# Kernel tuning notes

Measured on AMD Instinct MI355X. Metric: run time of the kernel, lower is better.

The kernel has to match this reference:

```python
import jax, jax.numpy as jnp
import numpy as np

IN_F, OUT_F, RANK = 4096, 4096, 4
ALPHA = 16
SCALING = ALPHA / RANK  # 4.0
B, L = 2, 4096


def setup_inputs() -> dict:
    key = jax.random.key(0)
    k_x, k_w, k_a, k_b = jax.random.split(key, 4)
    x = jax.random.normal(k_x, (B, L, IN_F), dtype=jnp.float32)
    W = jax.random.normal(k_w, (OUT_F, IN_F), dtype=jnp.float32) * 0.02
    # module inits lora_A ~ N(0, 1/rank), lora_B = zeros; we use small random B
    # so the low-rank branch is numerically active for kernel testing.
    lora_A = jax.random.normal(k_a, (RANK, IN_F), dtype=jnp.float32) * (1.0 / RANK)
    lora_B = jax.random.normal(k_b, (OUT_F, RANK), dtype=jnp.float32) * 0.02
    return {"x": x, "W": W, "lora_A": lora_A, "lora_B": lora_B}


def reference(x, W, lora_A, lora_B):
    # out = x @ W.T + ((x @ A.T) @ B.T) * scaling
    original = jnp.einsum('bli,oi->blo', x, W)
    lora_a = jnp.einsum('bli,ri->blr', x, lora_A)      # [B,L,rank]
    lora = jnp.einsum('blr,or->blo', lora_a, lora_B)   # [B,L,out]
    return original + lora * SCALING
```

## Files before the change

### kernel.cpp

```cpp
#include <hip/hip_runtime.h>
#include <stdint.h>

typedef signed char i8;
typedef unsigned char u8;
typedef __attribute__((ext_vector_type(4))) int i32x4;
typedef __attribute__((ext_vector_type(4))) float f32x4;

__device__ __forceinline__ void gload_lds16(const void* g, void* l) {
  __builtin_amdgcn_global_load_lds(
      (__attribute__((address_space(1))) void*)const_cast<void*>(g),
      (__attribute__((address_space(3))) void*)l, 16, 0, 0);
}

__global__ __launch_bounds__(256) void k_quant_x(const float* __restrict__ in,
                                                 i8* __restrict__ out,
                                                 float* __restrict__ scale) {
  const int row = blockIdx.x, t = threadIdx.x;
  const float* src = in + (size_t)row * 4096;
  float4 v[4];
  float m = 0.f;
#pragma unroll
  for (int j = 0; j < 4; ++j) {
    v[j] = *(const float4*)(src + j * 1024 + t * 4);
    m = fmaxf(m, fmaxf(fmaxf(fabsf(v[j].x), fabsf(v[j].y)),
                       fmaxf(fabsf(v[j].z), fabsf(v[j].w))));
  }
#pragma unroll
  for (int off = 32; off; off >>= 1) m = fmaxf(m, __shfl_xor(m, off));
  __shared__ float wmax[4];
  if ((t & 63) == 0) wmax[t >> 6] = m;
  __syncthreads();
  m = fmaxf(fmaxf(wmax[0], wmax[1]), fmaxf(wmax[2], wmax[3]));
  const float inv = m > 0.f ? 127.f / m : 0.f;
  if (t == 0) scale[row] = m / 127.f;
#pragma unroll
  for (int j = 0; j < 4; ++j) {
    int q0 = (int)rintf(fmaxf(fminf(v[j].x * inv, 127.f), -127.f));
    int q1 = (int)rintf(fmaxf(fminf(v[j].y * inv, 127.f), -127.f));
    int q2 = (int)rintf(fmaxf(fminf(v[j].z * inv, 127.f), -127.f));
    int q3 = (int)rintf(fmaxf(fminf(v[j].w * inv, 127.f), -127.f));
    uint32_t p = (q0 & 255) | ((q1 & 255) << 8) | ((q2 & 255) << 16) | ((q3 & 255) << 24);
    *(uint32_t*)(out + (size_t)row * 4096 + j * 1024 + t * 4) = p;
  }
}

__global__ __launch_bounds__(256) void k_quant_w(const float* __restrict__ W,
                                                 const float* __restrict__ Am,
                                                 const float* __restrict__ Bm,
                                                 i8* __restrict__ out,
                                                 float* __restrict__ scale) {
  const int o = blockIdx.x, t = threadIdx.x;
  const float4 b4 = *(const float4*)(Bm + (o << 2));
  float4 v[4];
  float m = 0.f;
#pragma unroll
  for (int j = 0; j < 4; ++j) {
    const int i = j * 1024 + t * 4;
    float4 w  = *(const float4*)(W + ((size_t)o << 12) + i);
    float4 a0 = *(const float4*)(Am + i);
    float4 a1 = *(const float4*)(Am + 4096 + i);
    float4 a2 = *(const float4*)(Am + 8192 + i);
    float4 a3 = *(const float4*)(Am + 12288 + i);
    w.x += 4.f * (b4.x * a0.x + b4.y * a1.x + b4.z * a2.x + b4.w * a3.x);
    w.y += 4.f * (b4.x * a0.y + b4.y * a1.y + b4.z * a2.y + b4.w * a3.y);
    w.z += 4.f * (b4.x * a0.z + b4.y * a1.z + b4.z * a2.z + b4.w * a3.z);
    w.w += 4.f * (b4.x * a0.w + b4.y * a1.w + b4.z * a2.w + b4.w * a3.w);
    v[j] = w;
    m = fmaxf(m, fmaxf(fmaxf(fabsf(w.x), fabsf(w.y)), fmaxf(fabsf(w.z), fabsf(w.w))));
  }
#pragma unroll
  for (int off = 32; off; off >>= 1) m = fmaxf(m, __shfl_xor(m, off));
  __shared__ float wmax[4];
  if ((t & 63) == 0) wmax[t >> 6] = m;
  __syncthreads();
  m = fmaxf(fmaxf(wmax[0], wmax[1]), fmaxf(wmax[2], wmax[3]));
  const float inv = m > 0.f ? 127.f / m : 0.f;
  if (t == 0) scale[o] = m / 127.f;
#pragma unroll
  for (int j = 0; j < 4; ++j) {
    int q0 = (int)rintf(fmaxf(fminf(v[j].x * inv, 127.f), -127.f));
    int q1 = (int)rintf(fmaxf(fminf(v[j].y * inv, 127.f), -127.f));
    int q2 = (int)rintf(fmaxf(fminf(v[j].z * inv, 127.f), -127.f));
    int q3 = (int)rintf(fmaxf(fminf(v[j].w * inv, 127.f), -127.f));
    uint32_t p = (q0 & 255) | ((q1 & 255) << 8) | ((q2 & 255) << 16) | ((q3 & 255) << 24);
    *(uint32_t*)(out + (size_t)o * 4096 + j * 1024 + t * 4) = p;
  }
}

__global__ __launch_bounds__(512, 2) void k_gq8(const u8* __restrict__ Ag,
                                                const u8* __restrict__ Bg,
                                                const float* __restrict__ sx,
                                                const float* __restrict__ sw,
                                                float* __restrict__ C,
                                                int M, int N, int K) {
  __shared__ __attribute__((aligned(16))) u8 As[2 * 32768];
  __shared__ __attribute__((aligned(16))) u8 Bs[2 * 32768];
  const int tid  = threadIdx.x;
  const int wave = tid >> 6, lane = tid & 63;
  const int wr = wave >> 2, wc = wave & 3;
  const int m0 = blockIdx.y * 256, n0 = blockIdx.x * 256;
  const int NT = K >> 7;

  const int srow = tid >> 3;
  const int csrc = (tid & 7) ^ (srow & 7);
  const u8* pA = Ag + (size_t)(m0 + srow) * K + csrc * 16;
  const u8* pB = Bg + (size_t)(n0 + srow) * K + csrc * 16;
  const size_t KH = (size_t)128 * K;
  const size_t KU = (size_t)64 * K;
  const int wb = wave << 10;

#define SA(nb, h, kt)                                                          \
  do {                                                                         \
    gload_lds16(pA + (h) * KH + (kt),      As + (nb) * 32768 + (h) * 16384 + wb);       \
    gload_lds16(pA + (h) * KH + KU + (kt), As + (nb) * 32768 + (h) * 16384 + 8192 + wb);\
  } while (0)
#define SB(nb, h, kt)                                                          \
  do {                                                                         \
    gload_lds16(pB + (h) * KH + (kt),      Bs + (nb) * 32768 + (h) * 16384 + wb);       \
    gload_lds16(pB + (h) * KH + KU + (kt), Bs + (nb) * 32768 + (h) * 16384 + 8192 + wb);\
  } while (0)

  const int l4 = lane & 15, q = lane >> 4, l7 = lane & 7;
  const int ke0 = (q ^ l7) << 4;
  const int aoff = ((wr << 6) + l4) << 7;
  const int boff = ((wc << 5) + l4) << 7;

  i32x4 acc[8][4] = {};
  i32x4 ar[4][2];
  i32x4 bq[2][2][2];

#define LDA(buf, mh)                                                           \
  do {                                                                         \
    const u8* b_ = As + (buf) * 32768 + (mh) * 16384 + aoff;                   \
    _Pragma("unroll") for (int f = 0; f < 4; ++f) {                            \
      ar[f][0] = *(const i32x4*)(b_ + f * 2048 + ke0);                         \
      ar[f][1] = *(const i32x4*)(b_ + f * 2048 + (ke0 ^ 64));                  \
    }                                                                          \
  } while (0)
#define LDB(buf, nh)                                                           \
  do {                                                                         \
    const u8* b_ = Bs + (buf) * 32768 + (nh) * 16384 + boff;                   \
    _Pragma("unroll") for (int g = 0; g < 2; ++g) {                            \
      bq[nh][g][0] = *(const i32x4*)(b_ + g * 2048 + ke0);                     \
      bq[nh][g][1] = *(const i32x4*)(b_ + g * 2048 + (ke0 ^ 64));              \
    }                                                                          \
  } while (0)
#define MFMA16(mh, nh)                                                         \
  do {                                                                         \
    __builtin_amdgcn_s_setprio(1);                                             \
    _Pragma("unroll") for (int f = 0; f < 4; ++f)                              \
      _Pragma("unroll") for (int g = 0; g < 2; ++g)                            \
        _Pragma("unroll") for (int ks = 0; ks < 2; ++ks)                       \
          acc[(mh) * 4 + f][(nh) * 2 + g] =                                    \
              __builtin_amdgcn_mfma_i32_16x16x64_i8(                           \
                  ar[f][ks], bq[nh][g][ks], acc[(mh) * 4 + f][(nh) * 2 + g],   \
                  0, 0, 0);                                                    \
    __builtin_amdgcn_s_setprio(0);                                             \
  } while (0)

  SA(0, 0, 0);
  SB(0, 0, 0);
  SB(0, 1, 0);
  SA(0, 1, 0);
  asm volatile("s_waitcnt vmcnt(4)" ::: "memory");
  __builtin_amdgcn_s_barrier();

  for (int t = 0; t < NT; ++t) {
    const int buf = t & 1, nb = buf ^ 1;
    const int kt1 = (t + 1) << 7;
    const bool st = (t + 1) < NT;

    LDA(buf, 0);
    LDB(buf, 0);
    if (st) SA(nb, 0, kt1);
    asm volatile("s_waitcnt lgkmcnt(8)" ::: "memory");
    __builtin_amdgcn_s_barrier();
    asm volatile("s_waitcnt lgkmcnt(0)" ::: "memory");
    MFMA16(0, 0);
    if (st) { asm volatile("s_waitcnt vmcnt(4)" ::: "memory"); }
    else    { asm volatile("s_waitcnt vmcnt(2)" ::: "memory"); }
    __builtin_amdgcn_s_barrier();

    LDB(buf, 1);
    if (st) SB(nb, 0, kt1);
    __builtin_amdgcn_s_barrier();
    asm volatile("s_waitcnt lgkmcnt(0)" ::: "memory");
    MFMA16(0, 1);
    if (st) { asm volatile("s_waitcnt vmcnt(4)" ::: "memory"); }
    else    { asm volatile("s_waitcnt vmcnt(0)" ::: "memory"); }
    __builtin_amdgcn_s_barrier();

    LDA(buf, 1);
    if (st) SB(nb, 1, kt1);
    __builtin_amdgcn_s_barrier();
    asm volatile("s_waitcnt lgkmcnt(0)" ::: "memory");
    MFMA16(1, 1);
    __builtin_amdgcn_s_barrier();

    if (st) SA(nb, 1, kt1);
    __builtin_amdgcn_s_barrier();
    MFMA16(1, 0);
    if (st) { asm volatile("s_waitcnt vmcnt(4)" ::: "memory"); }
    __builtin_amdgcn_s_barrier();
  }

  float swv[4];
#pragma unroll
  for (int j = 0; j < 4; ++j)
    swv[j] = sw[n0 + (j >> 1) * 128 + wc * 32 + (j & 1) * 16 + l4];
#pragma unroll
  for (int i = 0; i < 8; ++i) {
    const int mh = i >> 2, f = i & 3;
    const int row = m0 + mh * 128 + wr * 64 + f * 16 + q * 4;
#pragma unroll
    for (int j = 0; j < 4; ++j) {
      const int nh = j >> 1, g = j & 1;
      const int col = n0 + nh * 128 + wc * 32 + g * 16 + l4;
#pragma unroll
      for (int v = 0; v < 4; ++v)
        C[(size_t)(row + v) * N + col] = (float)acc[i][j][v] * sx[row + v] * swv[j];
    }
  }
#undef SA
#undef SB
#undef LDA
#undef LDB
#undef MFMA16
}

__global__ __launch_bounds__(256) void k_fallback(const float* __restrict__ X,
                                                  const float* __restrict__ W,
                                                  const float* __restrict__ Am,
                                                  const float* __restrict__ Bm,
                                                  float* __restrict__ C,
                                                  int M, int N, int K) {
  __shared__ float Xs[64][16];
  __shared__ float Ws[64][17];
  const int tid = threadIdx.x;
  const int tn = tid & 15, tm = tid >> 4;
  const int m0 = blockIdx.y * 64, n0 = blockIdx.x * 64;
  float acc[4][4] = {};
  for (int kt = 0; kt < K; kt += 16) {
    __syncthreads();
#pragma unroll
    for (int qq = 0; qq < 4; ++qq) {
      int idx = qq * 256 + tid;
      int r = idx >> 4, c = idx & 15;
      Xs[r][c] = X[(size_t)(m0 + r) * K + kt + c];
      float w = W[(size_t)(n0 + r) * K + kt + c];
      float4 b = *(const float4*)(Bm + ((n0 + r) << 2));
      w += 4.f * (b.x * Am[kt + c] + b.y * Am[4096 + kt + c] +
                  b.z * Am[8192 + kt + c] + b.w * Am[12288 + kt + c]);
      Ws[r][c] = w;
    }
    __syncthreads();
#pragma unroll
    for (int k = 0; k < 16; ++k) {
      float xv[4], wv[4];
#pragma unroll
      for (int i = 0; i < 4; ++i) xv[i] = Xs[tm * 4 + i][k];
#pragma unroll
      for (int j = 0; j < 4; ++j) wv[j] = Ws[tn * 4 + j][k];
#pragma unroll
      for (int i = 0; i < 4; ++i)
#pragma unroll
        for (int j = 0; j < 4; ++j) acc[i][j] += xv[i] * wv[j];
    }
  }
#pragma unroll
  for (int i = 0; i < 4; ++i)
#pragma unroll
    for (int j = 0; j < 4; ++j)
      C[(size_t)(m0 + tm * 4 + i) * N + n0 + tn * 4 + j] = acc[i][j];
}

extern "C" void kernel_launch(void* const* d_in, const int* in_sizes, int n_in,
                              void* d_out, int out_size, void* d_ws, size_t ws_size,
                              hipStream_t stream) {
  const float* x  = (const float*)d_in[0];
  const float* W  = (const float*)d_in[1];
  const float* lA = (const float*)d_in[2];
  const float* lB = (const float*)d_in[3];
  float* out = (float*)d_out;
  const int K = 4096, N = 4096;
  const int M = in_sizes[0] / K;
  const size_t need = (size_t)(M + N) * K + (size_t)(M + N) * sizeof(float);

  if (ws_size >= need && (M % 256) == 0) {
    i8* xb = (i8*)d_ws;
    i8* wb = xb + (size_t)M * K;
    float* sx = (float*)(wb + (size_t)N * K);
    float* sw = sx + M;
    k_quant_x<<<dim3(M), dim3(256), 0, stream>>>(x, xb, sx);
    k_quant_w<<<dim3(N), dim3(256), 0, stream>>>(W, lA, lB, wb, sw);
    k_gq8<<<dim3(N / 256, M / 256), dim3(512), 0, stream>>>(
        (const u8*)xb, (const u8*)wb, sx, sw, out, M, N, K);
  } else {
    k_fallback<<<dim3(N / 64, M / 64), dim3(256), 0, stream>>>(x, W, lA, lB, out, M, N, K);
  }
}
```

Measured before the change: 194.4 us.

## Merge x and W quantization kernels and swizzle GEMM workgroups across XCDs

Combines the separate activation and weight quantization kernels into one launch whose blocks branch on block index, removing one kernel launch and the tail gap between the two. The int8 GEMM now remaps its linear workgroup id so consecutive ids are spread in chunks of eight, aiming to place neighbouring tiles on the same XCD for better L2 reuse of shared A/B rows. A divisibility-by-eight guard is added to the fast path. The branchy fused quant kernel adds some divergence per block but no per-thread divergence.

```diff
diff --git a/kernel.cpp b/kernel.cpp
--- a/kernel.cpp
+++ b/kernel.cpp
@@ -4,7 +4,6 @@
 typedef signed char i8;
 typedef unsigned char u8;
 typedef __attribute__((ext_vector_type(4))) int i32x4;
-typedef __attribute__((ext_vector_type(4))) float f32x4;
 
 __device__ __forceinline__ void gload_lds16(const void* g, void* l) {
   __builtin_amdgcn_global_load_lds(
@@ -12,18 +11,44 @@
       (__attribute__((address_space(3))) void*)l, 16, 0, 0);
 }
 
-__global__ __launch_bounds__(256) void k_quant_x(const float* __restrict__ in,
-                                                 i8* __restrict__ out,
-                                                 float* __restrict__ scale) {
-  const int row = blockIdx.x, t = threadIdx.x;
-  const float* src = in + (size_t)row * 4096;
+__global__ __launch_bounds__(256) void k_quant(const float* __restrict__ x,
+                                               const float* __restrict__ W,
+                                               const float* __restrict__ Am,
+                                               const float* __restrict__ Bm,
+                                               i8* __restrict__ xq,
+                                               i8* __restrict__ wq,
+                                               float* __restrict__ sx,
+                                               float* __restrict__ sw, int M) {
+  const int bid = blockIdx.x, t = threadIdx.x;
+  const bool isx = bid < M;
+  const int row = isx ? bid : bid - M;
   float4 v[4];
   float m = 0.f;
-#pragma unroll
-  for (int j = 0; j < 4; ++j) {
-    v[j] = *(const float4*)(src + j * 1024 + t * 4);
-    m = fmaxf(m, fmaxf(fmaxf(fabsf(v[j].x), fabsf(v[j].y)),
-                       fmaxf(fabsf(v[j].z), fabsf(v[j].w))));
+  if (isx) {
+    const float4* src = (const float4*)(x + (size_t)row * 4096);
+#pragma unroll
+    for (int j = 0; j < 4; ++j) {
+      v[j] = src[j * 256 + t];
+      m = fmaxf(m, fmaxf(fmaxf(fabsf(v[j].x), fabsf(v[j].y)),
+                         fmaxf(fabsf(v[j].z), fabsf(v[j].w))));
+    }
+  } else {
+    const float4 b4 = *(const float4*)(Bm + (row << 2));
+#pragma unroll
+    for (int j = 0; j < 4; ++j) {
+      const int i = (j * 256 + t) * 4;
+      float4 w  = *(const float4*)(W + ((size_t)row << 12) + i);
+      float4 a0 = *(const float4*)(Am + i);
+      float4 a1 = *(const float4*)(Am + 4096 + i);
+      float4 a2 = *(const float4*)(Am + 8192 + i);
+      float4 a3 = *(const float4*)(Am + 12288 + i);
+      w.x += 4.f * (b4.x * a0.x + b4.y * a1.x + b4.z * a2.x + b4.w * a3.x);
+      w.y += 4.f * (b4.x * a0.y + b4.y * a1.y + b4.z * a2.y + b4.w * a3.y);
+      w.z += 4.f * (b4.x * a0.z + b4.y * a1.z + b4.z * a2.z + b4.w * a3.z);
+      w.w += 4.f * (b4.x * a0.w + b4.y * a1.w + b4.z * a2.w + b4.w * a3.w);
+      v[j] = w;
+      m = fmaxf(m, fmaxf(fmaxf(fabsf(w.x), fabsf(w.y)), fmaxf(fabsf(w.z), fabsf(w.w))));
+    }
   }
 #pragma unroll
   for (int off = 32; off; off >>= 1) m = fmaxf(m, __shfl_xor(m, off));
@@ -32,7 +57,8 @@
   __syncthreads();
   m = fmaxf(fmaxf(wmax[0], wmax[1]), fmaxf(wmax[2], wmax[3]));
   const float inv = m > 0.f ? 127.f / m : 0.f;
-  if (t == 0) scale[row] = m / 127.f;
+  if (t == 0) { if (isx) sx[row] = m / 127.f; else sw[row] = m / 127.f; }
+  i8* out = isx ? xq : wq;
 #pragma unroll
   for (int j = 0; j < 4; ++j) {
     int q0 = (int)rintf(fmaxf(fminf(v[j].x * inv, 127.f), -127.f));
@@ -40,50 +66,7 @@
     int q2 = (int)rintf(fmaxf(fminf(v[j].z * inv, 127.f), -127.f));
     int q3 = (int)rintf(fmaxf(fminf(v[j].w * inv, 127.f), -127.f));
     uint32_t p = (q0 & 255) | ((q1 & 255) << 8) | ((q2 & 255) << 16) | ((q3 & 255) << 24);
-    *(uint32_t*)(out + (size_t)row * 4096 + j * 1024 + t * 4) = p;
-  }
-}
-
-__global__ __launch_bounds__(256) void k_quant_w(const float* __restrict__ W,
-                                                 const float* __restrict__ Am,
-                                                 const float* __restrict__ Bm,
-                                                 i8* __restrict__ out,
-                                                 float* __restrict__ scale) {
-  const int o = blockIdx.x, t = threadIdx.x;
-  const float4 b4 = *(const float4*)(Bm + (o << 2));
-  float4 v[4];
-  float m = 0.f;
-#pragma unroll
-  for (int j = 0; j < 4; ++j) {
-    const int i = j * 1024 + t * 4;
-    float4 w  = *(const float4*)(W + ((size_t)o << 12) + i);
-    float4 a0 = *(const float4*)(Am + i);
-    float4 a1 = *(const float4*)(Am + 4096 + i);
-    float4 a2 = *(const float4*)(Am + 8192 + i);
-    float4 a3 = *(const float4*)(Am + 12288 + i);
-    w.x += 4.f * (b4.x * a0.x + b4.y * a1.x + b4.z * a2.x + b4.w * a3.x);
-    w.y += 4.f * (b4.x * a0.y + b4.y * a1.y + b4.z * a2.y + b4.w * a3.y);
-    w.z += 4.f * (b4.x * a0.z + b4.y * a1.z + b4.z * a2.z + b4.w * a3.z);
-    w.w += 4.f * (b4.x * a0.w + b4.y * a1.w + b4.z * a2.w + b4.w * a3.w);
-    v[j] = w;
-    m = fmaxf(m, fmaxf(fmaxf(fabsf(w.x), fabsf(w.y)), fmaxf(fabsf(w.z), fabsf(w.w))));
-  }
-#pragma unroll
-  for (int off = 32; off; off >>= 1) m = fmaxf(m, __shfl_xor(m, off));
-  __shared__ float wmax[4];
-  if ((t & 63) == 0) wmax[t >> 6] = m;
-  __syncthreads();
-  m = fmaxf(fmaxf(wmax[0], wmax[1]), fmaxf(wmax[2], wmax[3]));
-  const float inv = m > 0.f ? 127.f / m : 0.f;
-  if (t == 0) scale[o] = m / 127.f;
-#pragma unroll
-  for (int j = 0; j < 4; ++j) {
-    int q0 = (int)rintf(fmaxf(fminf(v[j].x * inv, 127.f), -127.f));
-    int q1 = (int)rintf(fmaxf(fminf(v[j].y * inv, 127.f), -127.f));
-    int q2 = (int)rintf(fmaxf(fminf(v[j].z * inv, 127.f), -127.f));
-    int q3 = (int)rintf(fmaxf(fminf(v[j].w * inv, 127.f), -127.f));
-    uint32_t p = (q0 & 255) | ((q1 & 255) << 8) | ((q2 & 255) << 16) | ((q3 & 255) << 24);
-    *(uint32_t*)(out + (size_t)o * 4096 + j * 1024 + t * 4) = p;
+    *(uint32_t*)(out + (size_t)row * 4096 + (j * 256 + t) * 4) = p;
   }
 }
 
@@ -98,8 +81,14 @@
   const int tid  = threadIdx.x;
   const int wave = tid >> 6, lane = tid & 63;
   const int wr = wave >> 2, wc = wave & 3;
-  const int m0 = blockIdx.y * 256, n0 = blockIdx.x * 256;
   const int NT = K >> 7;
+
+  const int gx = gridDim.x;
+  const int nwg = gx * gridDim.y;
+  const int orig = blockIdx.y * gx + blockIdx.x;
+  const int swz = (orig & 7) * (nwg >> 3) + (orig >> 3);
+  const int m0 = (swz / gx) * 256;
+  const int n0 = (swz % gx) * 256;
 
   const int srow = tid >> 3;
   const int csrc = (tid & 7) ^ (srow & 7);
@@ -285,14 +274,14 @@
   const int K = 4096, N = 4096;
   const int M = in_sizes[0] / K;
   const size_t need = (size_t)(M + N) * K + (size_t)(M + N) * sizeof(float);
-
-  if (ws_size >= need && (M % 256) == 0) {
+  const int nwg = (N / 256) * (M / 256);
+
+  if (ws_size >= need && (M % 256) == 0 && (nwg % 8) == 0) {
     i8* xb = (i8*)d_ws;
     i8* wb = xb + (size_t)M * K;
     float* sx = (float*)(wb + (size_t)N * K);
     float* sw = sx + M;
-    k_quant_x<<<dim3(M), dim3(256), 0, stream>>>(x, xb, sx);
-    k_quant_w<<<dim3(N), dim3(256), 0, stream>>>(W, lA, lB, wb, sw);
+    k_quant<<<dim3(M + N), dim3(256), 0, stream>>>(x, W, lA, lB, xb, wb, sx, sw, M);
     k_gq8<<<dim3(N / 256, M / 256), dim3(512), 0, stream>>>(
         (const u8*)xb, (const u8*)wb, sx, sw, out, M, N, K);
   } else {
```

After: 192.7 us. No clear change (-0.9%).
